# Kernel optimization log

Measured on AMD Instinct MI355X. Metric: run time of the kernel, lower is better.

Reference implementation:

```python
import jax, jax.numpy as jnp
import numpy as np

B, C, CE, H, W = 4, 128, 64, 64, 64
V = H * W
# parent(i) < i//2 guarantees depth <= ceil(log2(V)) = 12; 14 is a safe static bound
MAX_LEVELS = 14


def _gather_v(x, idx):
    # x: [B, C, V], idx: [B, V] -> gather along vertex dim (broadcast over C)
    return jnp.take_along_axis(x, idx[:, None, :], axis=2)


def _tree_filter(feature_in, embed_in, sorted_index, sorted_parent, node_level):
    Bv, Cv, Hv, Wv = feature_in.shape
    Vv = Hv * Wv
    f = feature_in.reshape(Bv, Cv, Vv)
    e = embed_in.reshape(Bv, embed_in.shape[1], Vv)
    # build_edge_weight: gather to BFS order, gather parent, squared-L2 distance, exp(-d)
    f_s = _gather_v(f, sorted_index)          # [B,C,V] features in topological order
    e_s = _gather_v(e, sorted_index)
    e_p = _gather_v(e_s, sorted_parent)
    d2 = jnp.sum((e_s - e_p) ** 2, axis=1)    # [B,V]
    w = jnp.exp(-d2)                          # edge weight node->parent (root: exp(0)=1, unused)
    wB = w[:, None, :]
    # ---- up sweep (leaves -> root), level-parallel over BFS levels ----
    # A_i = f_i + sum_{c in child(i)} w_c * A_c ; Z_i = 1 + sum w_c * Z_c (self_weight = 1)
    aggr_up = f_s
    nrm_up = jnp.ones((Bv, Vv), feature_in.dtype)
    for d in range(MAX_LEVELS - 1, 0, -1):
        mw = jnp.where(node_level == d, w, jnp.zeros((), feature_in.dtype))
        aggr_up = jax.vmap(lambda a, p, m: a.at[:, p].add(m))(
            aggr_up, sorted_parent, mw[:, None, :] * aggr_up)
        nrm_up = jax.vmap(lambda a, p, m: a.at[p].add(m))(
            nrm_up, sorted_parent, mw * nrm_up)
    # ---- down sweep (root -> leaves) ----
    # Ahat_i = A_i + w_i * (Ahat_parent - w_i * A_i); root keeps A_root
    aggr = aggr_up
    nrm = nrm_up
    for d in range(1, MAX_LEVELS):
        sel = node_level == d
        pa = _gather_v(aggr, sorted_parent)
        aggr = jnp.where(sel[:, None, :], aggr_up + wB * (pa - wB * aggr_up), aggr)
        pn = jnp.take_along_axis(nrm, sorted_parent, axis=1)
        nrm = jnp.where(sel, nrm_up + w * (pn - w * nrm_up), nrm)
    out_s = aggr / nrm[:, None, :]
    # scatter back from BFS order to original vertex order
    out = jax.vmap(lambda o, i: jnp.zeros_like(o).at[:, i].set(o))(out_s, sorted_index)
    return out.reshape(Bv, Cv, Hv, Wv)


def setup_inputs() -> dict:
    key = jax.random.key(0)
    k1, k2 = jax.random.split(key)
    feature_in = jax.random.normal(k1, (B, C, H, W), dtype=jnp.float32)
    embed_in = 0.1 * jax.random.normal(k2, (B, CE, H, W), dtype=jnp.float32)
    rng = np.random.default_rng(0)
    sorted_index = np.stack([rng.permutation(V) for _ in range(B)]).astype(np.int32)
    sorted_parent = np.zeros((B, V), dtype=np.int32)
    node_level = np.zeros((B, V), dtype=np.int32)
    for b in range(B):
        for i in range(1, V):
            p = int(rng.integers(0, max(1, i // 2)))  # parent earlier in order, depth <= log2(V)
            sorted_parent[b, i] = p
            node_level[b, i] = node_level[b, p] + 1
    return {
        "feature_in": feature_in,
        "embed_in": embed_in,
        "sorted_index": jnp.asarray(sorted_index),
        "sorted_parent": jnp.asarray(sorted_parent),
        "node_level": jnp.asarray(node_level),
    }


def reference(feature_in, embed_in, sorted_index, sorted_parent, node_level):
    return _tree_filter(feature_in, embed_in, sorted_index, sorted_parent, node_level)
```

## Files before the change

kernel.cpp:

```cpp
#include <hip/hip_runtime.h>

#define BB 4
#define CC 128
#define CE 64
#define VV 4096
#define NLEV 14


__device__ __forceinline__ void lds_fadd(float* p, float v) {
    unsafeAtomicAdd(p, v);
}

__global__ __launch_bounds__(256) void weight_kernel(
    const float* __restrict__ embed,
    const int* __restrict__ sorted_index,
    const int* __restrict__ sorted_parent,
    float* __restrict__ wsort)
{
    __shared__ float part[4][64];
    int bb   = blockIdx.x;
    int b    = bb >> 6;
    int n0   = (bb & 63) << 6;
    int lane = threadIdx.x & 63;
    int w    = threadIdx.x >> 6;
    int i    = n0 + lane;
    int vi = sorted_index[b * VV + i];
    int p  = sorted_parent[b * VV + i];
    int vp = sorted_index[b * VV + p];
    const float* eb = embed + (size_t)b * CE * VV;
    float acc = 0.f;
    #pragma unroll
    for (int r = 0; r < 16; ++r) {
        int ce = w * 16 + r;
        float d = eb[ce * VV + vi] - eb[ce * VV + vp];
        acc = fmaf(d, d, acc);
    }
    part[w][lane] = acc;
    __syncthreads();
    if (w == 0) {
        float d2 = part[0][lane] + part[1][lane] + part[2][lane] + part[3][lane];
        wsort[b * VV + i] = __expf(-d2);
    }
}

__global__ __launch_bounds__(256) void sortnrm_kernel(
    const int* __restrict__ sorted_index,
    const int* __restrict__ sorted_parent,
    const int* __restrict__ node_level,
    const float* __restrict__ wsort,
    int* __restrict__ giInv,
    int2* __restrict__ pw,
    float* __restrict__ inr,
    int* __restrict__ offs)
{
    __shared__ int   si_s[VV];
    __shared__ int   pos_s[VV];
    __shared__ int   lo_s[VV];
    __shared__ int   cp_s[VV];
    __shared__ float w_s[VV];
    __shared__ float vn[VV];
    __shared__ int hist[NLEV + 1];
    __shared__ int cursor[NLEV];
    __shared__ int offS[NLEV + 1];
    int b = blockIdx.x, tid = threadIdx.x;
    const int* lev = node_level    + b * VV;
    const int* si  = sorted_index  + b * VV;
    const int* par = sorted_parent + b * VV;

    if (tid < NLEV + 1) hist[tid] = 0;
    __syncthreads();
    for (int i = tid; i < VV; i += 256) {
        si_s[i] = si[i];
        int d = lev[i]; d = d < NLEV - 1 ? d : NLEV - 1;
        atomicAdd(&hist[d], 1);
    }
    __syncthreads();
    if (tid == 0) {
        int acc = 0;
        for (int d = 0; d < NLEV; ++d) { int h = hist[d]; offS[d] = acc; cursor[d] = acc; acc += h; }
        offS[NLEV] = acc;
    }
    __syncthreads();
    if (tid <= NLEV) offs[b * 16 + tid] = offS[tid];
    for (int i = tid; i < VV; i += 256) {
        int d = lev[i]; d = d < NLEV - 1 ? d : NLEV - 1;
        int k = atomicAdd(&cursor[d], 1);
        pos_s[i] = k;
        lo_s[k]  = i;
        giInv[b * VV + si_s[i]] = k;
    }
    __syncthreads();
    for (int k = tid; k < VV; k += 256) {
        int i = lo_s[k];
        cp_s[k] = pos_s[par[i]];
        w_s[k]  = wsort[b * VV + i];
        vn[k]   = 1.0f;
    }
    __syncthreads();
    for (int k = tid; k < VV; k += 256)
        pw[b * VV + k] = make_int2(cp_s[k], __float_as_int(w_s[k]));
    for (int d = NLEV - 1; d >= 1; --d) {
        int s = offS[d], e = offS[d + 1];
        if (s == e) continue;
        for (int k = s + tid; k < e; k += 256)
            lds_fadd(&vn[cp_s[k]], w_s[k] * vn[k]);
        __syncthreads();
    }
    for (int d = 1; d <= NLEV - 1; ++d) {
        int s = offS[d], e = offS[d + 1];
        if (s == e) continue;
        for (int k = s + tid; k < e; k += 256) {
            float u = vn[k], wk = w_s[k];
            vn[k] = fmaf(wk, fmaf(-wk, u, vn[cp_s[k]]), u);
        }
        __syncthreads();
    }
    for (int k = tid; k < VV; k += 256)
        inr[b * VV + k] = 1.0f / vn[k];
}

__global__ __launch_bounds__(256) void tree_kernel(
    const float* __restrict__ feat,
    const int* __restrict__ giInv,
    const int2* __restrict__ pw,
    const float* __restrict__ inr,
    const int* __restrict__ offs,
    float* __restrict__ out)
{
    __shared__ float val[VV];
    __shared__ int2  pwS[VV];
    __shared__ float inrS[VV];
    __shared__ int   offS[16];
    int b   = blockIdx.x >> 7;
    int c   = blockIdx.x & (CC - 1);
    int tid = threadIdx.x;

    const int2*  pwB = pw    + b * VV;
    const int*   ivB = giInv + b * VV;
    const float* inB = inr   + b * VV;
    const float* f   = feat + ((size_t)(b * CC + c)) * VV;

    if (tid < 16) offS[tid] = offs[b * 16 + tid];

    #pragma unroll
    for (int t = 0; t < 8; ++t) {
        int idx = tid + t * 256;
        ((int4*)pwS)[idx] = ((const int4*)pwB)[idx];
    }
    #pragma unroll
    for (int t = 0; t < 4; ++t) {
        int idx = tid + t * 256;
        ((float4*)inrS)[idx] = ((const float4*)inB)[idx];
    }

    #pragma unroll
    for (int t = 0; t < 4; ++t) {
        int idx = tid + t * 256;
        float4 fv = ((const float4*)f)[idx];
        int4   kk = ((const int4*)ivB)[idx];
        val[kk.x] = fv.x; val[kk.y] = fv.y; val[kk.z] = fv.z; val[kk.w] = fv.w;
    }
    __syncthreads();

    for (int d = NLEV - 1; d >= 1; --d) {
        int s = offS[d], e = offS[d + 1];
        if (s == e) continue;
        for (int k = s + tid; k < e; k += 256) {
            int2 cw = pwS[k];
            lds_fadd(&val[cw.x], __int_as_float(cw.y) * val[k]);
        }
        __syncthreads();
    }

    for (int d = 1; d <= NLEV - 1; ++d) {
        int s = offS[d], e = offS[d + 1];
        if (s == e) continue;
        for (int k = s + tid; k < e; k += 256) {
            int2 cw = pwS[k];
            float w = __int_as_float(cw.y);
            float u = val[k];
            val[k] = fmaf(w, fmaf(-w, u, val[cw.x]), u);
        }
        __syncthreads();
    }

    float* ob = out + ((size_t)(b * CC + c)) * VV;
    #pragma unroll
    for (int t = 0; t < 4; ++t) {
        int idx = tid + t * 256;
        int4 kk = ((const int4*)ivB)[idx];
        float4 r;
        r.x = val[kk.x] * inrS[kk.x];
        r.y = val[kk.y] * inrS[kk.y];
        r.z = val[kk.z] * inrS[kk.z];
        r.w = val[kk.w] * inrS[kk.w];
        ((float4*)ob)[idx] = r;
    }
}

extern "C" void kernel_launch(void* const* d_in, const int* in_sizes, int n_in,
                              void* d_out, int out_size, void* d_ws, size_t ws_size,
                              hipStream_t stream) {
    const float* feat          = (const float*)d_in[0];
    const float* embed         = (const float*)d_in[1];
    const int*   sorted_index  = (const int*)d_in[2];
    const int*   sorted_parent = (const int*)d_in[3];
    const int*   node_level    = (const int*)d_in[4];
    float* out = (float*)d_out;

    char* ws = (char*)d_ws;
    const size_t A = (size_t)BB * VV * 4;
    float* wsort = (float*)(ws);
    int*   giInv = (int*)  (ws + A);
    int2*  pw    = (int2*) (ws + 2 * A);
    float* inr   = (float*)(ws + 4 * A);
    int*   offs  = (int*)  (ws + 5 * A);

    weight_kernel<<<BB * 64, 256, 0, stream>>>(
        embed, sorted_index, sorted_parent, wsort);

    sortnrm_kernel<<<BB, 256, 0, stream>>>(
        sorted_index, sorted_parent, node_level, wsort, giInv, pw, inr, offs);

    tree_kernel<<<BB * CC, 256, 0, stream>>>(
        feat, giInv, pw, inr, offs, out);
}
```

Measured before the change: 118.3 us.

## Merge weight and sort kernels, fold normalizer sweep into per-channel tree kernel

The edge-weight computation and the level sort now run as different block ranges of one prep kernel, so one launch and one serial dependency disappear. The separate per-batch normalizer sweep is removed. Each channel block instead carries the normalizer alongside the feature as a float2 and divides at the end. The tree kernel goes to 512 threads and gathers weights from wsort via the stored original index. This trades a serial 4-block kernel for redundant normalizer work in every channel block, with double the LDS atomics per sweep.

```diff
diff --git a/kernel.cpp b/kernel.cpp
--- a/kernel.cpp
+++ b/kernel.cpp
@@ -11,189 +11,174 @@
     unsafeAtomicAdd(p, v);
 }
 
-__global__ __launch_bounds__(256) void weight_kernel(
+__global__ __launch_bounds__(256) void prep_kernel(
     const float* __restrict__ embed,
     const int* __restrict__ sorted_index,
     const int* __restrict__ sorted_parent,
-    float* __restrict__ wsort)
+    const int* __restrict__ node_level,
+    float* __restrict__ wsort,
+    int*   __restrict__ giInv,
+    int2*  __restrict__ cpl,
+    int*   __restrict__ offs)
 {
-    __shared__ float part[4][64];
-    int bb   = blockIdx.x;
-    int b    = bb >> 6;
-    int n0   = (bb & 63) << 6;
-    int lane = threadIdx.x & 63;
-    int w    = threadIdx.x >> 6;
-    int i    = n0 + lane;
-    int vi = sorted_index[b * VV + i];
-    int p  = sorted_parent[b * VV + i];
-    int vp = sorted_index[b * VV + p];
-    const float* eb = embed + (size_t)b * CE * VV;
-    float acc = 0.f;
-    #pragma unroll
-    for (int r = 0; r < 16; ++r) {
-        int ce = w * 16 + r;
-        float d = eb[ce * VV + vi] - eb[ce * VV + vp];
-        acc = fmaf(d, d, acc);
-    }
-    part[w][lane] = acc;
+    int tid = threadIdx.x;
+    if (blockIdx.x < BB) {
+        int b = blockIdx.x;
+        __shared__ int si_s[VV];
+        __shared__ int pos_s[VV];
+        __shared__ int lo_s[VV];
+        __shared__ int hist[NLEV + 1];
+        __shared__ int cursor[NLEV];
+        __shared__ int offSh[NLEV + 1];
+        const int* lev = node_level    + b * VV;
+        const int* si  = sorted_index  + b * VV;
+        const int* par = sorted_parent + b * VV;
+
+        if (tid < NLEV + 1) hist[tid] = 0;
+        __syncthreads();
+        for (int i = tid; i < VV; i += 256) {
+            si_s[i] = si[i];
+            int d = lev[i]; d = d < NLEV - 1 ? d : NLEV - 1;
+            atomicAdd(&hist[d], 1);
+        }
+        __syncthreads();
+        if (tid == 0) {
+            int acc = 0;
+            for (int d = 0; d < NLEV; ++d) { int h = hist[d]; offSh[d] = acc; cursor[d] = acc; acc += h; }
+            offSh[NLEV] = acc;
+        }
+        __syncthreads();
+        if (tid <= NLEV) offs[b * 16 + tid] = offSh[tid];
+        for (int i = tid; i < VV; i += 256) {
+            int d = lev[i]; d = d < NLEV - 1 ? d : NLEV - 1;
+            int k = atomicAdd(&cursor[d], 1);
+            pos_s[i] = k;
+            lo_s[k]  = i;
+            giInv[b * VV + si_s[i]] = k;
+        }
+        __syncthreads();
+        for (int k = tid; k < VV; k += 256) {
+            int i = lo_s[k];
+            cpl[b * VV + k] = make_int2(pos_s[par[i]], i);
+        }
+    } else {
+        __shared__ float part[4][64];
+        int bb   = blockIdx.x - BB;
+        int b    = bb >> 6;
+        int n0   = (bb & 63) << 6;
+        int lane = tid & 63;
+        int w    = tid >> 6;
+        int i    = n0 + lane;
+        int vi = sorted_index[b * VV + i];
+        int p  = sorted_parent[b * VV + i];
+        int vp = sorted_index[b * VV + p];
+        const float* eb = embed + (size_t)b * CE * VV;
+        float acc = 0.f;
+        #pragma unroll
+        for (int r = 0; r < 16; ++r) {
+            int ce = w * 16 + r;
+            float d = eb[ce * VV + vi] - eb[ce * VV + vp];
+            acc = fmaf(d, d, acc);
+        }
+        part[w][lane] = acc;
+        __syncthreads();
+        if (w == 0) {
+            float d2 = part[0][lane] + part[1][lane] + part[2][lane] + part[3][lane];
+            wsort[b * VV + i] = __expf(-d2);
+        }
+    }
+}
+
+__global__ __launch_bounds__(512) void tree_kernel(
+    const float* __restrict__ feat,
+    const float* __restrict__ wsort,
+    const int*  __restrict__ giInv,
+    const int2* __restrict__ cpl,
+    const int*  __restrict__ offs,
+    float* __restrict__ out)
+{
+    __shared__ float2 vv[VV];
+    __shared__ int2   cw[VV];
+    __shared__ int    offS[16];
+    int b   = blockIdx.x >> 7;
+    int c   = blockIdx.x & (CC - 1);
+    int tid = threadIdx.x;
+
+    const int2*  cplB = cpl   + b * VV;
+    const int*   ivB  = giInv + b * VV;
+    const float* wsB  = wsort + b * VV;
+    const float* f    = feat + ((size_t)(b * CC + c)) * VV;
+
+    if (tid < 16) offS[tid] = offs[b * 16 + tid];
+
+    #pragma unroll
+    for (int t = 0; t < 4; ++t) {
+        int idx = tid + t * 512;
+        ((int4*)cw)[idx] = ((const int4*)cplB)[idx];
+    }
+
+    int4 kkR[2];
+    #pragma unroll
+    for (int t = 0; t < 2; ++t) {
+        int idx = tid + t * 512;
+        float4 fv = ((const float4*)f)[idx];
+        int4   kk = ((const int4*)ivB)[idx];
+        kkR[t] = kk;
+        vv[kk.x] = make_float2(fv.x, 1.f);
+        vv[kk.y] = make_float2(fv.y, 1.f);
+        vv[kk.z] = make_float2(fv.z, 1.f);
+        vv[kk.w] = make_float2(fv.w, 1.f);
+    }
     __syncthreads();
-    if (w == 0) {
-        float d2 = part[0][lane] + part[1][lane] + part[2][lane] + part[3][lane];
-        wsort[b * VV + i] = __expf(-d2);
-    }
-}
-
-__global__ __launch_bounds__(256) void sortnrm_kernel(
-    const int* __restrict__ sorted_index,
-    const int* __restrict__ sorted_parent,
-    const int* __restrict__ node_level,
-    const float* __restrict__ wsort,
-    int* __restrict__ giInv,
-    int2* __restrict__ pw,
-    float* __restrict__ inr,
-    int* __restrict__ offs)
-{
-    __shared__ int   si_s[VV];
-    __shared__ int   pos_s[VV];
-    __shared__ int   lo_s[VV];
-    __shared__ int   cp_s[VV];
-    __shared__ float w_s[VV];
-    __shared__ float vn[VV];
-    __shared__ int hist[NLEV + 1];
-    __shared__ int cursor[NLEV];
-    __shared__ int offS[NLEV + 1];
-    int b = blockIdx.x, tid = threadIdx.x;
-    const int* lev = node_level    + b * VV;
-    const int* si  = sorted_index  + b * VV;
-    const int* par = sorted_parent + b * VV;
-
-    if (tid < NLEV + 1) hist[tid] = 0;
+
+    #pragma unroll
+    for (int t = 0; t < 8; ++t) {
+        int k = tid + t * 512;
+        cw[k].y = __float_as_int(wsB[cw[k].y]);
+    }
     __syncthreads();
-    for (int i = tid; i < VV; i += 256) {
-        si_s[i] = si[i];
-        int d = lev[i]; d = d < NLEV - 1 ? d : NLEV - 1;
-        atomicAdd(&hist[d], 1);
-    }
-    __syncthreads();
-    if (tid == 0) {
-        int acc = 0;
-        for (int d = 0; d < NLEV; ++d) { int h = hist[d]; offS[d] = acc; cursor[d] = acc; acc += h; }
-        offS[NLEV] = acc;
-    }
-    __syncthreads();
-    if (tid <= NLEV) offs[b * 16 + tid] = offS[tid];
-    for (int i = tid; i < VV; i += 256) {
-        int d = lev[i]; d = d < NLEV - 1 ? d : NLEV - 1;
-        int k = atomicAdd(&cursor[d], 1);
-        pos_s[i] = k;
-        lo_s[k]  = i;
-        giInv[b * VV + si_s[i]] = k;
-    }
-    __syncthreads();
-    for (int k = tid; k < VV; k += 256) {
-        int i = lo_s[k];
-        cp_s[k] = pos_s[par[i]];
-        w_s[k]  = wsort[b * VV + i];
-        vn[k]   = 1.0f;
-    }
-    __syncthreads();
-    for (int k = tid; k < VV; k += 256)
-        pw[b * VV + k] = make_int2(cp_s[k], __float_as_int(w_s[k]));
+
     for (int d = NLEV - 1; d >= 1; --d) {
         int s = offS[d], e = offS[d + 1];
         if (s == e) continue;
-        for (int k = s + tid; k < e; k += 256)
-            lds_fadd(&vn[cp_s[k]], w_s[k] * vn[k]);
-        __syncthreads();
-    }
+        for (int k = s + tid; k < e; k += 512) {
+            int2 x = cw[k];
+            float w = __int_as_float(x.y);
+            float2 u = vv[k];
+            lds_fadd(&vv[x.x].x, w * u.x);
+            lds_fadd(&vv[x.x].y, w * u.y);
+        }
+        __syncthreads();
+    }
+
     for (int d = 1; d <= NLEV - 1; ++d) {
         int s = offS[d], e = offS[d + 1];
         if (s == e) continue;
-        for (int k = s + tid; k < e; k += 256) {
-            float u = vn[k], wk = w_s[k];
-            vn[k] = fmaf(wk, fmaf(-wk, u, vn[cp_s[k]]), u);
-        }
-        __syncthreads();
-    }
-    for (int k = tid; k < VV; k += 256)
-        inr[b * VV + k] = 1.0f / vn[k];
-}
-
-__global__ __launch_bounds__(256) void tree_kernel(
-    const float* __restrict__ feat,
-    const int* __restrict__ giInv,
-    const int2* __restrict__ pw,
-    const float* __restrict__ inr,
-    const int* __restrict__ offs,
-    float* __restrict__ out)
-{
-    __shared__ float val[VV];
-    __shared__ int2  pwS[VV];
-    __shared__ float inrS[VV];
-    __shared__ int   offS[16];
-    int b   = blockIdx.x >> 7;
-    int c   = blockIdx.x & (CC - 1);
-    int tid = threadIdx.x;
-
-    const int2*  pwB = pw    + b * VV;
-    const int*   ivB = giInv + b * VV;
-    const float* inB = inr   + b * VV;
-    const float* f   = feat + ((size_t)(b * CC + c)) * VV;
-
-    if (tid < 16) offS[tid] = offs[b * 16 + tid];
-
-    #pragma unroll
-    for (int t = 0; t < 8; ++t) {
-        int idx = tid + t * 256;
-        ((int4*)pwS)[idx] = ((const int4*)pwB)[idx];
-    }
-    #pragma unroll
-    for (int t = 0; t < 4; ++t) {
-        int idx = tid + t * 256;
-        ((float4*)inrS)[idx] = ((const float4*)inB)[idx];
-    }
-
-    #pragma unroll
-    for (int t = 0; t < 4; ++t) {
-        int idx = tid + t * 256;
-        float4 fv = ((const float4*)f)[idx];
-        int4   kk = ((const int4*)ivB)[idx];
-        val[kk.x] = fv.x; val[kk.y] = fv.y; val[kk.z] = fv.z; val[kk.w] = fv.w;
-    }
-    __syncthreads();
-
-    for (int d = NLEV - 1; d >= 1; --d) {
-        int s = offS[d], e = offS[d + 1];
-        if (s == e) continue;
-        for (int k = s + tid; k < e; k += 256) {
-            int2 cw = pwS[k];
-            lds_fadd(&val[cw.x], __int_as_float(cw.y) * val[k]);
-        }
-        __syncthreads();
-    }
-
-    for (int d = 1; d <= NLEV - 1; ++d) {
-        int s = offS[d], e = offS[d + 1];
-        if (s == e) continue;
-        for (int k = s + tid; k < e; k += 256) {
-            int2 cw = pwS[k];
-            float w = __int_as_float(cw.y);
-            float u = val[k];
-            val[k] = fmaf(w, fmaf(-w, u, val[cw.x]), u);
+        for (int k = s + tid; k < e; k += 512) {
+            int2 x = cw[k];
+            float w = __int_as_float(x.y);
+            float2 u  = vv[k];
+            float2 pa = vv[x.x];
+            vv[k] = make_float2(fmaf(w, fmaf(-w, u.x, pa.x), u.x),
+                                fmaf(w, fmaf(-w, u.y, pa.y), u.y));
         }
         __syncthreads();
     }
 
     float* ob = out + ((size_t)(b * CC + c)) * VV;
     #pragma unroll
-    for (int t = 0; t < 4; ++t) {
-        int idx = tid + t * 256;
-        int4 kk = ((const int4*)ivB)[idx];
+    for (int t = 0; t < 2; ++t) {
+        int idx = tid + t * 512;
+        int4 kk = kkR[t];
+        float2 u0 = vv[kk.x];
+        float2 u1 = vv[kk.y];
+        float2 u2 = vv[kk.z];
+        float2 u3 = vv[kk.w];
         float4 r;
-        r.x = val[kk.x] * inrS[kk.x];
-        r.y = val[kk.y] * inrS[kk.y];
-        r.z = val[kk.z] * inrS[kk.z];
-        r.w = val[kk.w] * inrS[kk.w];
+        r.x = __fdividef(u0.x, u0.y);
+        r.y = __fdividef(u1.x, u1.y);
+        r.z = __fdividef(u2.x, u2.y);
+        r.w = __fdividef(u3.x, u3.y);
         ((float4*)ob)[idx] = r;
     }
 }
@@ -212,16 +197,12 @@
     const size_t A = (size_t)BB * VV * 4;
     float* wsort = (float*)(ws);
     int*   giInv = (int*)  (ws + A);
-    int2*  pw    = (int2*) (ws + 2 * A);
-    float* inr   = (float*)(ws + 4 * A);
-    int*   offs  = (int*)  (ws + 5 * A);
-
-    weight_kernel<<<BB * 64, 256, 0, stream>>>(
-        embed, sorted_index, sorted_parent, wsort);
-
-    sortnrm_kernel<<<BB, 256, 0, stream>>>(
-        sorted_index, sorted_parent, node_level, wsort, giInv, pw, inr, offs);
-
-    tree_kernel<<<BB * CC, 256, 0, stream>>>(
-        feat, giInv, pw, inr, offs, out);
-}
+    int2*  cpl   = (int2*) (ws + 2 * A);
+    int*   offs  = (int*)  (ws + 4 * A);
+
+    prep_kernel<<<BB + BB * 64, 256, 0, stream>>>(
+        embed, sorted_index, sorted_parent, node_level, wsort, giInv, cpl, offs);
+
+    tree_kernel<<<BB * CC, 512, 0, stream>>>(
+        feat, wsort, giInv, cpl, offs, out);
+}
```

After: 115.9 us. -2.0%, faster.
